# Optimization experiments

Measured on AMD Instinct MI355X. Metric: run time of the kernel, lower is better.

## Reference

```python
import jax, jax.numpy as jnp
import numpy as np
from jax.scipy.special import gammaln

D_MODEL = 256
N_HEADS = 8
BIAS_HIDDEN = 64
B, N = 2, 1024
EPS = 1e-4


def setup_inputs() -> dict:
    key = jax.random.key(0)
    ks = jax.random.split(key, 12)
    d, h = D_MODEL, BIAS_HIDDEN
    s = 0.02
    return {
        "src": jax.random.normal(ks[0], (B, N, d), jnp.float32),
        "coords": jax.random.normal(ks[1], (B, N, 4), jnp.float32),
        "Wq": jax.random.normal(ks[2], (d, d), jnp.float32) * s,
        "Wk": jax.random.normal(ks[3], (d, d), jnp.float32) * s,
        "Wv": jax.random.normal(ks[4], (d, d), jnp.float32) * s,
        "Wo": jax.random.normal(ks[5], (d, d), jnp.float32) * s,
        "gw1": jax.random.normal(ks[6], (h, 2), jnp.float32) * s,
        "gb1": jnp.zeros((h,), jnp.float32),
        "gw2": jax.random.normal(ks[7], (1, h), jnp.float32) * s,
        "gb2": jnp.zeros((1,), jnp.float32),
        "dw1": jax.random.normal(ks[8], (h, 4), jnp.float32) * s,
        "db1": jnp.zeros((h,), jnp.float32),
        "dw2": jax.random.normal(ks[9], (2, h), jnp.float32) * s,
        "db2": jnp.zeros((2,), jnp.float32),
    }


def reference(src, coords, Wq, Wk, Wv, Wo, gw1, gb1, gw2, gb2, dw1, db1, dw2, db2):
    Bb, Nn, d = src.shape
    H = N_HEADS
    dh = d // H
    scale = 1.0 / np.sqrt(dh).astype(np.float32)

    def split_heads(x):  # [B,N,d] -> [B,H,N,dh]
        return x.reshape(Bb, Nn, H, dh).transpose(0, 2, 1, 3)

    q = split_heads(src @ Wq.T)
    k = split_heads(src @ Wk.T)
    v = split_heads(src @ Wv.T)

    attn = jnp.einsum("bhnd,bhmd->bhnm", q, k) * scale  # [B,H,N,N]

    xyz = coords[..., :3]
    t = coords[..., 3]
    delta = xyz[:, :, None, :] - xyz[:, None, :, :]        # [B,N,N,3]
    dist = jnp.linalg.norm(delta, axis=-1)                  # [B,N,N]
    dt = t[:, :, None] - t[:, None, :]                      # [B,N,N]

    # geometric bias MLP: 2 -> hidden -> 1
    geom_feat = jnp.stack((dist, dt), axis=-1)              # [B,N,N,2]
    gh = jax.nn.relu(geom_feat @ gw1.T + gb1)
    bias = (gh @ gw2.T + gb2)[..., 0]                       # [B,N,N]

    # delay bias MLP: [dist, xyz_j] (4) -> hidden -> 2 (Gamma shape, rate)
    xyz_j = jnp.broadcast_to(xyz[:, None, :, :], (Bb, Nn, Nn, 3))
    delay_feat = jnp.concatenate((dist[..., None], xyz_j), axis=-1)  # [B,N,N,4]
    dhid = jax.nn.relu(delay_feat @ dw1.T + db1)
    raw = dhid @ dw2.T + db2                                # [B,N,N,2]
    shape = jax.nn.softplus(raw[..., 0]) + EPS
    rate = jax.nn.softplus(raw[..., 1]) + EPS
    dt_pos = jnp.maximum(jnp.abs(dt), EPS)
    # Gamma(shape, rate).log_prob(x)
    log_prob = (shape * jnp.log(rate) + (shape - 1.0) * jnp.log(dt_pos)
                - rate * dt_pos - gammaln(shape))
    bias = bias + log_prob

    attn = attn + bias[:, None, :, :]
    weights = jax.nn.softmax(attn, axis=-1)
    out = jnp.einsum("bhnm,bhmd->bhnd", weights, v)
    out = out.transpose(0, 2, 1, 3).reshape(Bb, Nn, d)
    return out @ Wo.T
```

## Files before the change

### kernel.cpp

```cpp
#include <hip/hip_runtime.h>
#include <hip/hip_bf16.h>
#include <math.h>

constexpr int B_ = 2;
constexpr int N_ = 1024;
constexpr int D_ = 256;
constexpr int H_ = 8;
constexpr int DH_ = 32;
constexpr float SCALE_ = 0.17677669529663687f;
constexpr float LOG2E_ = 1.4426950408889634f;
constexpr float SCALE2_ = SCALE_ * LOG2E_;
constexpr float EPSV_ = 1e-4f;

typedef __attribute__((ext_vector_type(8))) short short8;
typedef __attribute__((ext_vector_type(4))) float f32x4;

__device__ __forceinline__ unsigned short f2bf(float x) {
  __hip_bfloat16 h = __float2bfloat16(x);
  return __builtin_bit_cast(unsigned short, h);
}
__device__ __forceinline__ float bf2f(unsigned short u) {
  unsigned int x = ((unsigned int)u) << 16;
  return __builtin_bit_cast(float, x);
}

__device__ __forceinline__ float lgamma_fast(float x) {
  float y = (x < 1.f) ? x : (x - 1.f);
  float g = fmaf(y, 0.035868343f, -0.193527818f);
  g = fmaf(y, g, 0.482199394f);
  g = fmaf(y, g, -0.756704078f);
  g = fmaf(y, g, 0.918206857f);
  g = fmaf(y, g, -0.897056937f);
  g = fmaf(y, g, 0.988205891f);
  g = fmaf(y, g, -0.577191652f);
  g = fmaf(y, g, 1.0f);
  float lg = __logf(g);
  return (x < 1.f) ? lg - __logf(x) : lg;
}
__device__ __forceinline__ float softplus_fast(float x) {
  return __logf(1.f + __expf(x));
}

__global__ __launch_bounds__(256)
void prep_kernel(const float* __restrict__ coords,
                 const float* __restrict__ gw1, const float* __restrict__ gb1,
                 const float* __restrict__ gw2, const float* __restrict__ gb2,
                 const float* __restrict__ dw1, const float* __restrict__ db1,
                 const float* __restrict__ dw2, const float* __restrict__ db2,
                 const float* __restrict__ Wq, const float* __restrict__ Wk,
                 const float* __restrict__ Wv, const float* __restrict__ Wo,
                 const float* __restrict__ src,
                 unsigned short* __restrict__ whi, unsigned short* __restrict__ wlo,
                 unsigned short* __restrict__ shi, unsigned short* __restrict__ slo,
                 float2* __restrict__ Gp, float4* __restrict__ Dp) {
  const int tid = threadIdx.x;
  const int bi = blockIdx.x;

  if (bi < 33) {
    int e = bi * 256 + tid;
    if (e < 129 * 64) {
      int kv = e >> 6, ku = e & 63;
      float v = kv * 0.25f - 16.0f;
      float u0 = ku * 0.25f, u1 = u0 + 0.25f;
      float a0 = gb2[0], a1 = gb2[0];
#pragma unroll 4
      for (int h = 0; h < 64; ++h) {
        float g0 = gw1[2 * h], g1 = gw1[2 * h + 1], gb = gb1[h], g2 = gw2[h];
        float base = fmaf(g1, v, gb);
        a0 = fmaf(g2, fmaxf(fmaf(g0, u0, base), 0.f), a0);
        a1 = fmaf(g2, fmaxf(fmaf(g0, u1, base), 0.f), a1);
      }
      Gp[e] = make_float2(a0, a1);
    }
    return;
  }

  if (bi < 545) {
    int t = (bi - 33) * 256 + tid;
    int b = t >> 16;
    int rem = t & 65535;
    int k = rem >> 10;
    int j = rem & 1023;
    float4 cj = ((const float4*)coords)[b * N_ + j];
    float u0 = k * 0.25f, u1 = u0 + 0.25f;
    float r00 = db2[0], r10 = db2[1], r01 = db2[0], r11 = db2[1];
#pragma unroll 4
    for (int h = 0; h < 64; ++h) {
      float w0 = dw1[4 * h], wx = dw1[4 * h + 1], wy = dw1[4 * h + 2], wz = dw1[4 * h + 3];
      float c0 = db1[h], c1 = dw2[h], c2 = dw2[64 + h];
      float dp = fmaf(wx, cj.x, fmaf(wy, cj.y, fmaf(wz, cj.z, c0)));
      float h0 = fmaxf(fmaf(w0, u0, dp), 0.f);
      float h1 = fmaxf(fmaf(w0, u1, dp), 0.f);
      r00 = fmaf(c1, h0, r00); r10 = fmaf(c2, h0, r10);
      r01 = fmaf(c1, h1, r01); r11 = fmaf(c2, h1, r11);
    }
    Dp[((size_t)b * 64 + k) * 1024 + j] = make_float4(r00, r10, r01, r11);
    return;
  }

  if (bi < 609) {
    int idx = ((bi - 545) * 256 + tid) * 16;
    int m = idx >> 16;
    int off = idx & 65535;
    const float* p = ((m == 0) ? Wq : (m == 1) ? Wk : (m == 2) ? Wv : Wo) + off;
    unsigned short* dhi = whi + idx;
    unsigned short* dlo = wlo + idx;
#pragma unroll
    for (int q = 0; q < 4; ++q) {
      float4 f = *(const float4*)(p + q * 4);
      ushort4 hi, lo;
      hi.x = f2bf(f.x); lo.x = f2bf(f.x - bf2f(hi.x));
      hi.y = f2bf(f.y); lo.y = f2bf(f.y - bf2f(hi.y));
      hi.z = f2bf(f.z); lo.z = f2bf(f.z - bf2f(hi.z));
      hi.w = f2bf(f.w); lo.w = f2bf(f.w - bf2f(hi.w));
      *(ushort4*)(dhi + q * 4) = hi;
      *(ushort4*)(dlo + q * 4) = lo;
    }
    return;
  }

  {
    int idx = ((bi - 609) * 256 + tid) * 16;
    const float* p = src + idx;
    unsigned short* dhi = shi + idx;
    unsigned short* dlo = slo + idx;
#pragma unroll
    for (int q = 0; q < 4; ++q) {
      float4 f = *(const float4*)(p + q * 4);
      ushort4 hi, lo;
      hi.x = f2bf(f.x); lo.x = f2bf(f.x - bf2f(hi.x));
      hi.y = f2bf(f.y); lo.y = f2bf(f.y - bf2f(hi.y));
      hi.z = f2bf(f.z); lo.z = f2bf(f.z - bf2f(hi.z));
      hi.w = f2bf(f.w); lo.w = f2bf(f.w - bf2f(hi.w));
      *(ushort4*)(dhi + q * 4) = hi;
      *(ushort4*)(dlo + q * 4) = lo;
    }
  }
}

__device__ __forceinline__
void mfma_wave_pure(const unsigned short* __restrict__ Ahi,
                    const unsigned short* __restrict__ Alo,
                    const unsigned short* __restrict__ whi,
                    const unsigned short* __restrict__ wlo,
                    int r0, int c0, f32x4 (&acc)[4]) {
  const int l = threadIdx.x & 63;
  const int lr = l & 15, lg = l >> 4;
#pragma unroll
  for (int ct = 0; ct < 4; ++ct) acc[ct] = (f32x4){0.f, 0.f, 0.f, 0.f};
#pragma unroll 2
  for (int ks = 0; ks < 8; ++ks) {
    size_t aoff = (size_t)(r0 + lr) * D_ + ks * 32 + lg * 8;
    short8 ahi = *(const short8*)(Ahi + aoff);
    short8 alo = *(const short8*)(Alo + aoff);
#pragma unroll
    for (int ct = 0; ct < 4; ++ct) {
      size_t woff = (size_t)(c0 + ct * 16 + lr) * D_ + ks * 32 + lg * 8;
      short8 wh = *(const short8*)(whi + woff);
      short8 wl = *(const short8*)(wlo + woff);
      acc[ct] = __builtin_amdgcn_mfma_f32_16x16x32_bf16(ahi, wh, acc[ct], 0, 0, 0);
      acc[ct] = __builtin_amdgcn_mfma_f32_16x16x32_bf16(alo, wh, acc[ct], 0, 0, 0);
      acc[ct] = __builtin_amdgcn_mfma_f32_16x16x32_bf16(ahi, wl, acc[ct], 0, 0, 0);
    }
  }
}

__global__ __launch_bounds__(256)
void fused1_kernel(const float* __restrict__ coords,
                   const float2* __restrict__ Gp, const float4* __restrict__ Dp,
                   float* __restrict__ bias,
                   const unsigned short* __restrict__ shi,
                   const unsigned short* __restrict__ slo,
                   const unsigned short* __restrict__ whi,
                   const unsigned short* __restrict__ wlo,
                   unsigned short* __restrict__ qbf, unsigned short* __restrict__ kbf,
                   unsigned short* __restrict__ vtbf) {
  const int tid = threadIdx.x;
  const int bi = blockIdx.x;

  if (bi >= 2048) {
    const int bi2 = bi - 2048;
    const int z = bi2 >> 7;
    const int rem = bi2 & 127;
    const int by = rem >> 5, bx = rem & 31;
    const int w = tid >> 6;
    const int r0 = bx * 64 + w * 16;
    const int c0 = by * 64;
    f32x4 acc[4];
    mfma_wave_pure(shi, slo, whi + z * 65536, wlo + z * 65536, r0, c0, acc);

    const int l = tid & 63, lr = l & 15, lg = l >> 4;
    if (z < 2) {
      unsigned short* dst = (z == 0) ? qbf : kbf;
#pragma unroll
      for (int ct = 0; ct < 4; ++ct) {
        int o = c0 + ct * 16 + lr, h = o >> 5, d = o & 31;
#pragma unroll
        for (int r = 0; r < 4; ++r) {
          int R = r0 + lg * 4 + r, b = R >> 10, n = R & 1023;
          dst[(size_t)((b * H_ + h) * N_ + n) * DH_ + d] = f2bf(acc[ct][r]);
        }
      }
    } else {
#pragma unroll
      for (int ct = 0; ct < 4; ++ct) {
        int o = c0 + ct * 16 + lr, h = o >> 5, d = o & 31;
#pragma unroll
        for (int r = 0; r < 4; ++r) {
          int R = r0 + lg * 4 + r, b = R >> 10, n = R & 1023;
          vtbf[(size_t)((b * H_ + h) * DH_ + d) * N_ + n] = f2bf(acc[ct][r]);
        }
      }
    }
    return;
  }

  const int jt = bi & 3;
  const int it = (bi >> 2) & 255;
  const int b  = bi >> 10;
  const int j  = jt * 256 + tid;
  const int ibase = it * 4;

  const float4 cj = ((const float4*)coords)[b * N_ + j];
  const float4* DpB = Dp + (size_t)b * 64 * 1024;

#pragma unroll
  for (int ii = 0; ii < 4; ++ii) {
    const float* cp = coords + 4 * (b * N_ + ibase + ii);
    float dx = cp[0] - cj.x, dy = cp[1] - cj.y, dz = cp[2] - cj.z;
    float dist = sqrtf(dx * dx + dy * dy + dz * dz);
    float dtv = cp[3] - cj.w;

    float uf = fminf(dist, 15.999f) * 4.0f;
    int ku = (int)uf;
    float fu = uf - (float)ku;
    float4 t = DpB[(size_t)ku * 1024 + j];
    float raw0 = fmaf(fu, t.z - t.x, t.x);
    float raw1 = fmaf(fu, t.w - t.y, t.y);

    float vf = (fminf(fmaxf(dtv, -16.0f), 15.999f) + 16.0f) * 4.0f;
    int kv = (int)vf;
    float fv = vf - (float)kv;
    float2 a = Gp[kv * 64 + ku];
    float2 c = Gp[(kv + 1) * 64 + ku];
    float gl = fmaf(fu, a.y - a.x, a.x);
    float gh = fmaf(fu, c.y - c.x, c.x);
    float biasg = fmaf(fv, gh - gl, gl);

    float sh  = softplus_fast(raw0) + EPSV_;
    float ra  = softplus_fast(raw1) + EPSV_;
    float dtp = fmaxf(fabsf(dtv), EPSV_);
    float lp  = sh * __logf(ra) + (sh - 1.f) * __logf(dtp) - ra * dtp - lgamma_fast(sh);
    bias[(size_t)(b * N_ + ibase + ii) * N_ + j] = (biasg + lp) * LOG2E_;
  }
}

__global__ __launch_bounds__(512)
void attn_kernel(const unsigned short* __restrict__ qbf,
                 const unsigned short* __restrict__ kbf,
                 const unsigned short* __restrict__ vtbf,
                 const float* __restrict__ biasg,
                 unsigned short* __restrict__ ophi,
                 unsigned short* __restrict__ oplo) {
  __shared__ __align__(16) unsigned short p_lds[8][16][72];
  __shared__ float acc_lds[3][2][16][32];
  __shared__ float l_lds[3][2][16];

  const int tid = threadIdx.x;
  const int w = tid >> 6, l = tid & 63;
  const int s = w >> 2, jq = w & 3;
  const int lr = l & 15, lg = l >> 4;
  const int bh = blockIdx.x >> 5;
  const int qb = blockIdx.x & 31;
  const int b = bh >> 3, h = bh & 7;
  const int ibase = qb * 32 + s * 16;

  const short8 ones8 = {16256, 16256, 16256, 16256, 16256, 16256, 16256, 16256};

  const short8 qfrag =
      *(const short8*)(qbf + (size_t)(bh * N_ + ibase + lr) * DH_ + lg * 8);
  const unsigned short* kb = kbf + (size_t)bh * N_ * DH_;
  const unsigned short* vb = vtbf + (size_t)bh * DH_ * N_;
  const float* bbase = biasg + (size_t)b * N_ * N_;

  f32x4 acc[2], accL;
  acc[0] = (f32x4){0.f, 0.f, 0.f, 0.f};
  acc[1] = (f32x4){0.f, 0.f, 0.f, 0.f};
  accL   = (f32x4){0.f, 0.f, 0.f, 0.f};

  const int jbeg = jq * 256;
  for (int j0 = jbeg; j0 < jbeg + 256; j0 += 64) {
    f32x4 sc[4];
#pragma unroll
    for (int t = 0; t < 4; ++t) {
      short8 kf = *(const short8*)(kb + (size_t)(j0 + t * 16 + lr) * DH_ + lg * 8);
      sc[t] = __builtin_amdgcn_mfma_f32_16x16x32_bf16(
          qfrag, kf, (f32x4){0.f, 0.f, 0.f, 0.f}, 0, 0, 0);
    }
#pragma unroll
    for (int r = 0; r < 4; ++r) {
      const float* bi = bbase + (size_t)(ibase + lg * 4 + r) * N_ + j0 + lr;
#pragma unroll
      for (int t = 0; t < 4; ++t)
        sc[t][r] = fmaf(sc[t][r], SCALE2_, bi[t * 16]);
    }
#pragma unroll
    for (int t = 0; t < 4; ++t)
#pragma unroll
      for (int r = 0; r < 4; ++r)
        p_lds[w][lg * 4 + r][t * 16 + lr] = f2bf(exp2f(sc[t][r]));
#pragma unroll
    for (int kc = 0; kc < 2; ++kc) {
      short8 pf = *(const short8*)&p_lds[w][lr][kc * 32 + lg * 8];
#pragma unroll
      for (int c = 0; c < 2; ++c) {
        short8 vf = *(const short8*)(vb + (size_t)(c * 16 + lr) * N_ +
                                     j0 + kc * 32 + lg * 8);
        acc[c] = __builtin_amdgcn_mfma_f32_16x16x32_bf16(pf, vf, acc[c], 0, 0, 0);
      }
      accL = __builtin_amdgcn_mfma_f32_16x16x32_bf16(pf, ones8, accL, 0, 0, 0);
    }
  }

  if (jq > 0) {
#pragma unroll
    for (int c = 0; c < 2; ++c)
#pragma unroll
      for (int r = 0; r < 4; ++r)
        acc_lds[jq - 1][s][lg * 4 + r][c * 16 + lr] = acc[c][r];
    if (lr == 0) {
#pragma unroll
      for (int r = 0; r < 4; ++r)
        l_lds[jq - 1][s][lg * 4 + r] = accL[r];
    }
  }
  __syncthreads();
  if (jq == 0) {
    float linv[4];
#pragma unroll
    for (int r = 0; r < 4; ++r) {
      int row = lg * 4 + r;
      float lsum = accL[r];
#pragma unroll
      for (int q = 0; q < 3; ++q) lsum += l_lds[q][s][row];
      linv[r] = 1.f / lsum;
    }
#pragma unroll
    for (int c = 0; c < 2; ++c) {
#pragma unroll
      for (int r = 0; r < 4; ++r) {
        int row = lg * 4 + r;
        int i = ibase + row;
        int d = c * 16 + lr;
        float o = acc[c][r];
#pragma unroll
        for (int q = 0; q < 3; ++q) o += acc_lds[q][s][row][d];
        o *= linv[r];
        size_t oidx = (size_t)(b * N_ + i) * D_ + h * DH_ + d;
        unsigned short hi = f2bf(o);
        ophi[oidx] = hi;
        oplo[oidx] = f2bf(o - bf2f(hi));
      }
    }
  }
}

__global__ __launch_bounds__(256)
void projo_kernel(const unsigned short* __restrict__ ophi,
                  const unsigned short* __restrict__ oplo,
                  const unsigned short* __restrict__ whi,
                  const unsigned short* __restrict__ wlo,
                  float* __restrict__ out) {
  const int w = threadIdx.x >> 6;
  const int r0 = blockIdx.x * 64 + w * 16;
  const int c0 = blockIdx.y * 64;
  f32x4 acc[4];
  mfma_wave_pure(ophi, oplo, whi + 3 * 65536, wlo + 3 * 65536, r0, c0, acc);
  const int l = threadIdx.x & 63, lr = l & 15, lg = l >> 4;
#pragma unroll
  for (int ct = 0; ct < 4; ++ct)
#pragma unroll
    for (int r = 0; r < 4; ++r)
      out[(size_t)(r0 + lg * 4 + r) * D_ + c0 + ct * 16 + lr] = acc[ct][r];
}

extern "C" void kernel_launch(void* const* d_in, const int* in_sizes, int n_in,
                              void* d_out, int out_size, void* d_ws, size_t ws_size,
                              hipStream_t stream) {
  const float* src    = (const float*)d_in[0];
  const float* coords = (const float*)d_in[1];
  const float* Wq  = (const float*)d_in[2];
  const float* Wk  = (const float*)d_in[3];
  const float* Wv  = (const float*)d_in[4];
  const float* Wo  = (const float*)d_in[5];
  const float* gw1 = (const float*)d_in[6];
  const float* gb1 = (const float*)d_in[7];
  const float* gw2 = (const float*)d_in[8];
  const float* gb2 = (const float*)d_in[9];
  const float* dw1 = (const float*)d_in[10];
  const float* db1 = (const float*)d_in[11];
  const float* dw2 = (const float*)d_in[12];
  const float* db2 = (const float*)d_in[13];
  float* out = (float*)d_out;

  char* wsb = (char*)d_ws;
  unsigned short* qbf  = (unsigned short*)wsb;
  unsigned short* kbf  = (unsigned short*)(wsb + (1 << 20));
  unsigned short* vtbf = (unsigned short*)(wsb + (2 << 20));
  float* biasw         = (float*)(wsb + (3 << 20));
  unsigned short* whi  = (unsigned short*)(wsb + (11 << 20));
  unsigned short* wlo  = (unsigned short*)(wsb + (11 << 20) + (512 << 10));
  unsigned short* shi  = (unsigned short*)(wsb + (12 << 20));
  unsigned short* slo  = (unsigned short*)(wsb + (13 << 20));
  unsigned short* ophi = (unsigned short*)(wsb + (14 << 20));
  unsigned short* oplo = (unsigned short*)(wsb + (15 << 20));
  float2* Gp           = (float2*)(wsb + (16 << 20));
  float4* Dp           = (float4*)(wsb + (17 << 20));

  prep_kernel<<<737, 256, 0, stream>>>(coords, gw1, gb1, gw2, gb2,
                                       dw1, db1, dw2, db2,
                                       Wq, Wk, Wv, Wo, src,
                                       whi, wlo, shi, slo, Gp, Dp);
  fused1_kernel<<<2432, 256, 0, stream>>>(coords, Gp, Dp, biasw,
                                          shi, slo, whi, wlo, qbf, kbf, vtbf);
  attn_kernel<<<512, 512, 0, stream>>>(qbf, kbf, vtbf, biasw, ophi, oplo);
  projo_kernel<<<dim3(32, 4), 256, 0, stream>>>(ophi, oplo, whi, wlo, out);
}
```

Measured before the change: 69.67 us.

## Fuse bf16 hi/lo splitting into QKV projection and move Wo split to fused1

```diff
diff --git a/kernel.cpp b/kernel.cpp
--- a/kernel.cpp
+++ b/kernel.cpp
@@ -22,6 +22,21 @@
 __device__ __forceinline__ float bf2f(unsigned short u) {
   unsigned int x = ((unsigned int)u) << 16;
   return __builtin_bit_cast(float, x);
+}
+
+__device__ __forceinline__ void split8(const float* __restrict__ p,
+                                       short8& hi, short8& lo) {
+  f32x4 f0 = *(const f32x4*)p;
+  f32x4 f1 = *(const f32x4*)(p + 4);
+#pragma unroll
+  for (int i = 0; i < 4; ++i) {
+    unsigned short h0 = f2bf(f0[i]);
+    hi[i] = (short)h0;
+    lo[i] = (short)f2bf(f0[i] - bf2f(h0));
+    unsigned short h1 = f2bf(f1[i]);
+    hi[4 + i] = (short)h1;
+    lo[4 + i] = (short)f2bf(f1[i] - bf2f(h1));
+  }
 }
 
 __device__ __forceinline__ float lgamma_fast(float x) {
@@ -47,36 +62,12 @@
                  const float* __restrict__ gw2, const float* __restrict__ gb2,
                  const float* __restrict__ dw1, const float* __restrict__ db1,
                  const float* __restrict__ dw2, const float* __restrict__ db2,
-                 const float* __restrict__ Wq, const float* __restrict__ Wk,
-                 const float* __restrict__ Wv, const float* __restrict__ Wo,
-                 const float* __restrict__ src,
-                 unsigned short* __restrict__ whi, unsigned short* __restrict__ wlo,
-                 unsigned short* __restrict__ shi, unsigned short* __restrict__ slo,
                  float2* __restrict__ Gp, float4* __restrict__ Dp) {
   const int tid = threadIdx.x;
   const int bi = blockIdx.x;
 
-  if (bi < 33) {
-    int e = bi * 256 + tid;
-    if (e < 129 * 64) {
-      int kv = e >> 6, ku = e & 63;
-      float v = kv * 0.25f - 16.0f;
-      float u0 = ku * 0.25f, u1 = u0 + 0.25f;
-      float a0 = gb2[0], a1 = gb2[0];
-#pragma unroll 4
-      for (int h = 0; h < 64; ++h) {
-        float g0 = gw1[2 * h], g1 = gw1[2 * h + 1], gb = gb1[h], g2 = gw2[h];
-        float base = fmaf(g1, v, gb);
-        a0 = fmaf(g2, fmaxf(fmaf(g0, u0, base), 0.f), a0);
-        a1 = fmaf(g2, fmaxf(fmaf(g0, u1, base), 0.f), a1);
-      }
-      Gp[e] = make_float2(a0, a1);
-    }
-    return;
-  }
-
-  if (bi < 545) {
-    int t = (bi - 33) * 256 + tid;
+  if (bi < 512) {
+    int t = bi * 256 + tid;
     int b = t >> 16;
     int rem = t & 65535;
     int k = rem >> 10;
@@ -98,42 +89,42 @@
     return;
   }
 
-  if (bi < 609) {
-    int idx = ((bi - 545) * 256 + tid) * 16;
-    int m = idx >> 16;
-    int off = idx & 65535;
-    const float* p = ((m == 0) ? Wq : (m == 1) ? Wk : (m == 2) ? Wv : Wo) + off;
-    unsigned short* dhi = whi + idx;
-    unsigned short* dlo = wlo + idx;
-#pragma unroll
-    for (int q = 0; q < 4; ++q) {
-      float4 f = *(const float4*)(p + q * 4);
-      ushort4 hi, lo;
-      hi.x = f2bf(f.x); lo.x = f2bf(f.x - bf2f(hi.x));
-      hi.y = f2bf(f.y); lo.y = f2bf(f.y - bf2f(hi.y));
-      hi.z = f2bf(f.z); lo.z = f2bf(f.z - bf2f(hi.z));
-      hi.w = f2bf(f.w); lo.w = f2bf(f.w - bf2f(hi.w));
-      *(ushort4*)(dhi + q * 4) = hi;
-      *(ushort4*)(dlo + q * 4) = lo;
-    }
-    return;
-  }
-
   {
-    int idx = ((bi - 609) * 256 + tid) * 16;
-    const float* p = src + idx;
-    unsigned short* dhi = shi + idx;
-    unsigned short* dlo = slo + idx;
-#pragma unroll
-    for (int q = 0; q < 4; ++q) {
-      float4 f = *(const float4*)(p + q * 4);
-      ushort4 hi, lo;
-      hi.x = f2bf(f.x); lo.x = f2bf(f.x - bf2f(hi.x));
-      hi.y = f2bf(f.y); lo.y = f2bf(f.y - bf2f(hi.y));
-      hi.z = f2bf(f.z); lo.z = f2bf(f.z - bf2f(hi.z));
-      hi.w = f2bf(f.w); lo.w = f2bf(f.w - bf2f(hi.w));
-      *(ushort4*)(dhi + q * 4) = hi;
-      *(ushort4*)(dlo + q * 4) = lo;
+    int e = (bi - 512) * 256 + tid;
+    if (e < 129 * 64) {
+      int kv = e >> 6, ku = e & 63;
+      float v = kv * 0.25f - 16.0f;
+      float u0 = ku * 0.25f, u1 = u0 + 0.25f;
+      float a0 = gb2[0], a1 = gb2[0];
+#pragma unroll 4
+      for (int h = 0; h < 64; ++h) {
+        float g0 = gw1[2 * h], g1 = gw1[2 * h + 1], gb = gb1[h], g2 = gw2[h];
+        float base = fmaf(g1, v, gb);
+        a0 = fmaf(g2, fmaxf(fmaf(g0, u0, base), 0.f), a0);
+        a1 = fmaf(g2, fmaxf(fmaf(g0, u1, base), 0.f), a1);
+      }
+      Gp[e] = make_float2(a0, a1);
+    }
+  }
+}
+
+__device__ __forceinline__
+void mfma_proj_wave_f32(const float* __restrict__ A, const float* __restrict__ W,
+                        int r0, int c0, int l, f32x4 (&acc)[4]) {
+  const int lr = l & 15, lg = l >> 4;
+#pragma unroll
+  for (int ct = 0; ct < 4; ++ct) acc[ct] = (f32x4){0.f, 0.f, 0.f, 0.f};
+#pragma unroll 2
+  for (int ks = 0; ks < 8; ++ks) {
+    short8 ahi, alo;
+    split8(A + (size_t)(r0 + lr) * D_ + ks * 32 + lg * 8, ahi, alo);
+#pragma unroll
+    for (int ct = 0; ct < 4; ++ct) {
+      short8 wh, wl;
+      split8(W + (size_t)(c0 + ct * 16 + lr) * D_ + ks * 32 + lg * 8, wh, wl);
+      acc[ct] = __builtin_amdgcn_mfma_f32_16x16x32_bf16(ahi, wh, acc[ct], 0, 0, 0);
+      acc[ct] = __builtin_amdgcn_mfma_f32_16x16x32_bf16(alo, wh, acc[ct], 0, 0, 0);
+      acc[ct] = __builtin_amdgcn_mfma_f32_16x16x32_bf16(ahi, wl, acc[ct], 0, 0, 0);
     }
   }
 }
@@ -169,25 +160,25 @@
 void fused1_kernel(const float* __restrict__ coords,
                    const float2* __restrict__ Gp, const float4* __restrict__ Dp,
                    float* __restrict__ bias,
-                   const unsigned short* __restrict__ shi,
-                   const unsigned short* __restrict__ slo,
-                   const unsigned short* __restrict__ whi,
-                   const unsigned short* __restrict__ wlo,
+                   const float* __restrict__ Wq, const float* __restrict__ Wk,
+                   const float* __restrict__ Wv, const float* __restrict__ Wo,
+                   const float* __restrict__ src,
+                   unsigned short* __restrict__ whi, unsigned short* __restrict__ wlo,
                    unsigned short* __restrict__ qbf, unsigned short* __restrict__ kbf,
                    unsigned short* __restrict__ vtbf) {
   const int tid = threadIdx.x;
   const int bi = blockIdx.x;
 
-  if (bi >= 2048) {
-    const int bi2 = bi - 2048;
-    const int z = bi2 >> 7;
-    const int rem = bi2 & 127;
+  if (bi < 384) {
+    const int z = bi >> 7;
+    const float* W = (z == 0) ? Wq : (z == 1) ? Wk : Wv;
+    const int rem = bi & 127;
     const int by = rem >> 5, bx = rem & 31;
     const int w = tid >> 6;
     const int r0 = bx * 64 + w * 16;
     const int c0 = by * 64;
     f32x4 acc[4];
-    mfma_wave_pure(shi, slo, whi + z * 65536, wlo + z * 65536, r0, c0, acc);
+    mfma_proj_wave_f32(src, W, r0, c0, tid & 63, acc);
 
     const int l = tid & 63, lr = l & 15, lg = l >> 4;
     if (z < 2) {
@@ -215,9 +206,23 @@
     return;
   }
 
-  const int jt = bi & 3;
-  const int it = (bi >> 2) & 255;
-  const int b  = bi >> 10;
+  if (bi < 448) {
+    int idx = ((bi - 384) * 256 + tid) * 4;
+    float4 f = *(const float4*)(Wo + idx);
+    ushort4 hi, lo;
+    hi.x = f2bf(f.x); lo.x = f2bf(f.x - bf2f(hi.x));
+    hi.y = f2bf(f.y); lo.y = f2bf(f.y - bf2f(hi.y));
+    hi.z = f2bf(f.z); lo.z = f2bf(f.z - bf2f(hi.z));
+    hi.w = f2bf(f.w); lo.w = f2bf(f.w - bf2f(hi.w));
+    *(ushort4*)(whi + idx) = hi;
+    *(ushort4*)(wlo + idx) = lo;
+    return;
+  }
+
+  const int u  = bi - 448;
+  const int jt = u & 3;
+  const int it = (u >> 2) & 255;
+  const int b  = u >> 10;
   const int j  = jt * 256 + tid;
   const int ibase = it * 4;
 
@@ -375,7 +380,7 @@
   const int r0 = blockIdx.x * 64 + w * 16;
   const int c0 = blockIdx.y * 64;
   f32x4 acc[4];
-  mfma_wave_pure(ophi, oplo, whi + 3 * 65536, wlo + 3 * 65536, r0, c0, acc);
+  mfma_wave_pure(ophi, oplo, whi, wlo, r0, c0, acc);
   const int l = threadIdx.x & 63, lr = l & 15, lg = l >> 4;
 #pragma unroll
   for (int ct = 0; ct < 4; ++ct)
@@ -409,20 +414,17 @@
   unsigned short* vtbf = (unsigned short*)(wsb + (2 << 20));
   float* biasw         = (float*)(wsb + (3 << 20));
   unsigned short* whi  = (unsigned short*)(wsb + (11 << 20));
-  unsigned short* wlo  = (unsigned short*)(wsb + (11 << 20) + (512 << 10));
-  unsigned short* shi  = (unsigned short*)(wsb + (12 << 20));
-  unsigned short* slo  = (unsigned short*)(wsb + (13 << 20));
+  unsigned short* wlo  = (unsigned short*)(wsb + (11 << 20) + (256 << 10));
   unsigned short* ophi = (unsigned short*)(wsb + (14 << 20));
   unsigned short* oplo = (unsigned short*)(wsb + (15 << 20));
   float2* Gp           = (float2*)(wsb + (16 << 20));
   float4* Dp           = (float4*)(wsb + (17 << 20));
 
-  prep_kernel<<<737, 256, 0, stream>>>(coords, gw1, gb1, gw2, gb2,
-                                       dw1, db1, dw2, db2,
-                                       Wq, Wk, Wv, Wo, src,
-                                       whi, wlo, shi, slo, Gp, Dp);
-  fused1_kernel<<<2432, 256, 0, stream>>>(coords, Gp, Dp, biasw,
-                                          shi, slo, whi, wlo, qbf, kbf, vtbf);
+  prep_kernel<<<545, 256, 0, stream>>>(coords, gw1, gb1, gw2, gb2,
+                                       dw1, db1, dw2, db2, Gp, Dp);
+  fused1_kernel<<<2496, 256, 0, stream>>>(coords, Gp, Dp, biasw,
+                                          Wq, Wk, Wv, Wo, src,
+                                          whi, wlo, qbf, kbf, vtbf);
   attn_kernel<<<512, 512, 0, stream>>>(qbf, kbf, vtbf, biasw, ophi, oplo);
   projo_kernel<<<dim3(32, 4), 256, 0, stream>>>(ophi, oplo, whi, wlo, out);
 }
```

Result: faster. 66.65 us (-4.3%).
